# Performance work log

Measured on AMD Instinct MI355X. Metric: run time of the kernel, lower is better.

## Reference

```python
import jax, jax.numpy as jnp
import numpy as np

NUM_EMBEDDINGS = 8192
EMBEDDING_DIM = 256


def setup_inputs() -> dict:
    key = jax.random.key(0)
    kx, kw = jax.random.split(key)
    x = jax.random.normal(kx, (16384, EMBEDDING_DIM), dtype=jnp.float32)
    # nn.Embedding weight initialized uniform(-1/K, 1/K)
    bound = 1.0 / NUM_EMBEDDINGS
    weight = jax.random.uniform(kw, (NUM_EMBEDDINGS, EMBEDDING_DIM),
                                dtype=jnp.float32, minval=-bound, maxval=bound)
    return {"x": x, "weight": weight}


def reference(x, weight):
    # flatten to (N, D)
    flat_x = x.reshape(-1, EMBEDDING_DIM)
    distances = (jnp.sum(flat_x * flat_x, axis=1, keepdims=True)
                 + jnp.sum(weight * weight, axis=1)
                 - 2.0 * jnp.matmul(flat_x, weight.T))
    encoding_indices = jnp.argmin(distances, axis=1)  # (N,)
    quantized = weight[encoding_indices].reshape(x.shape)
    return quantized, encoding_indices
```

## Files before the change

### kernel.cpp

```cpp
#include <hip/hip_runtime.h>
#include <hip/hip_bf16.h>

#define NROWS 16384
#define NCODES 8192
#define DIM 256
#define BM 128
#define CPB 4096
#define CAP 24
#define MARGIN 3.0e-4f

typedef __attribute__((ext_vector_type(8))) short bf16x8;
typedef __attribute__((ext_vector_type(4))) float f32x4;

__device__ inline unsigned short f2bf(float f) {
    union { __hip_bfloat16 h; unsigned short u; } cv;
    cv.h = __float2bfloat16(f);
    return cv.u;
}
__device__ inline unsigned f2ord(float f) {
    unsigned u = __float_as_uint(f);
    return u ^ ((u >> 31) ? 0xFFFFFFFFu : 0x80000000u);
}
__device__ inline float ord2f(unsigned u) {
    unsigned v = (u & 0x80000000u) ? (u ^ 0x80000000u) : ~u;
    return __uint_as_float(v);
}

__device__ float pairwise256_sq(const float4* p) {
    float res[2];
    #pragma unroll
    for (int h = 0; h < 2; ++h) {
        float r[8];
        #pragma unroll
        for (int j = 0; j < 8; ++j) r[j] = 0.0f;
        #pragma unroll
        for (int g = 0; g < 16; ++g) {
            float4 v0 = p[h * 32 + g * 2];
            float4 v1 = p[h * 32 + g * 2 + 1];
            r[0] = __fadd_rn(r[0], __fmul_rn(v0.x, v0.x));
            r[1] = __fadd_rn(r[1], __fmul_rn(v0.y, v0.y));
            r[2] = __fadd_rn(r[2], __fmul_rn(v0.z, v0.z));
            r[3] = __fadd_rn(r[3], __fmul_rn(v0.w, v0.w));
            r[4] = __fadd_rn(r[4], __fmul_rn(v1.x, v1.x));
            r[5] = __fadd_rn(r[5], __fmul_rn(v1.y, v1.y));
            r[6] = __fadd_rn(r[6], __fmul_rn(v1.z, v1.z));
            r[7] = __fadd_rn(r[7], __fmul_rn(v1.w, v1.w));
        }
        res[h] = __fadd_rn(__fadd_rn(__fadd_rn(r[0], r[1]), __fadd_rn(r[2], r[3])),
                           __fadd_rn(__fadd_rn(r[4], r[5]), __fadd_rn(r[6], r[7])));
    }
    return __fadd_rn(res[0], res[1]);
}

__global__ __launch_bounds__(256) void sq_kernel(const float* __restrict__ x,
                                                 const float* __restrict__ w,
                                                 float* __restrict__ xsq,
                                                 float* __restrict__ wsq) {
    int gid = blockIdx.x * 256 + threadIdx.x;
    if (gid < NROWS)
        xsq[gid] = pairwise256_sq(reinterpret_cast<const float4*>(x + (size_t)gid * DIM));
    else
        wsq[gid - NROWS] =
            pairwise256_sq(reinterpret_cast<const float4*>(w + (size_t)(gid - NROWS) * DIM));
}

__global__ __launch_bounds__(256) void wfrag_kernel(const float* __restrict__ w,
                                                    unsigned short* __restrict__ whf) {
    int tid = blockIdx.x * 256 + threadIdx.x;
    int L = tid & 63;
    int rest = tid >> 6;
    int c16 = rest & 511;
    int k32 = rest >> 9;
    int code = c16 * 16 + (L & 15);
    int k = k32 * 32 + (L >> 4) * 8;
    const float4* p = reinterpret_cast<const float4*>(w + (size_t)code * DIM + k);
    float4 u0 = p[0], u1 = p[1];
    unsigned short tmp[8];
    tmp[0] = f2bf(u0.x); tmp[1] = f2bf(u0.y); tmp[2] = f2bf(u0.z); tmp[3] = f2bf(u0.w);
    tmp[4] = f2bf(u1.x); tmp[5] = f2bf(u1.y); tmp[6] = f2bf(u1.z); tmp[7] = f2bf(u1.w);
    *reinterpret_cast<uint4*>(whf + (size_t)tid * 8) = *reinterpret_cast<uint4*>(tmp);
}

__global__ __launch_bounds__(512, 2)
void vq_main(const float* __restrict__ x, const float* __restrict__ w,
             const unsigned short* __restrict__ whf,
             const float* __restrict__ wsq, const float* __restrict__ xsq,
             unsigned long long* __restrict__ best64g) {
    __shared__ unsigned short afrag[8 * 8 * 64 * 8];
    __shared__ unsigned rowmin[BM];
    __shared__ int cnt[BM];
    __shared__ int cand[BM][CAP];

    const int tid = threadIdx.x;
    const int lane = tid & 63;
    const int wv = tid >> 6;
    const int lm = lane & 15;
    const int lq = lane >> 4;

    const int blk = blockIdx.x;
    const int xcd = blk & 7;
    const int split = xcd & 1;
    const int rowGroup = (xcd >> 1) * 32 + (blk >> 3);
    const int rowBase = rowGroup * BM;
    const int codeBase = split * CPB;

    if (tid < BM) { rowmin[tid] = 0xFFFFFFFFu; cnt[tid] = 0; }

    {
        const int rg = wv;
        const float* xr = x + (size_t)(rowBase + rg * 16 + lm) * DIM + lq * 8;
        #pragma unroll
        for (int k32 = 0; k32 < 8; ++k32) {
            float4 u0 = *reinterpret_cast<const float4*>(xr + k32 * 32);
            float4 u1 = *reinterpret_cast<const float4*>(xr + k32 * 32 + 4);
            unsigned short t8[8];
            t8[0] = f2bf(u0.x); t8[1] = f2bf(u0.y); t8[2] = f2bf(u0.z); t8[3] = f2bf(u0.w);
            t8[4] = f2bf(u1.x); t8[5] = f2bf(u1.y); t8[6] = f2bf(u1.z); t8[7] = f2bf(u1.w);
            *reinterpret_cast<uint4*>(afrag + ((rg * 8 + k32) * 64 + lane) * 8) =
                *reinterpret_cast<uint4*>(t8);
        }
    }
    __syncthreads();

    const int waveCode16 = (codeBase + wv * 512) >> 4;

    for (int p = 0; p < 8; ++p) {
        const int pbase16 = waveCode16 + p * 4;
        f32x4 acc[8][4];
        #pragma unroll
        for (int rg = 0; rg < 8; ++rg)
            #pragma unroll
            for (int cf = 0; cf < 4; ++cf)
                acc[rg][cf] = (f32x4){0.f, 0.f, 0.f, 0.f};

        bf16x8 bb[2][4];
        #pragma unroll
        for (int cf = 0; cf < 4; ++cf)
            bb[0][cf] = *reinterpret_cast<const bf16x8*>(
                whf + (((size_t)(pbase16 + cf)) * 64 + lane) * 8);

        #pragma unroll
        for (int k32 = 0; k32 < 8; ++k32) {
            const int cur = k32 & 1;
            if (k32 < 7) {
                #pragma unroll
                for (int cf = 0; cf < 4; ++cf)
                    bb[cur ^ 1][cf] = *reinterpret_cast<const bf16x8*>(
                        whf + (((size_t)((k32 + 1) * 512 + pbase16 + cf)) * 64 + lane) * 8);
            }
            bf16x8 a[8];
            #pragma unroll
            for (int rg = 0; rg < 8; ++rg)
                a[rg] = *reinterpret_cast<const bf16x8*>(
                    afrag + ((rg * 8 + k32) * 64 + lane) * 8);
            #pragma unroll
            for (int cf = 0; cf < 4; ++cf)
                #pragma unroll
                for (int rg = 0; rg < 8; ++rg)
                    acc[rg][cf] = __builtin_amdgcn_mfma_f32_16x16x32_bf16(
                        a[rg], bb[cur][cf], acc[rg][cf], 0, 0, 0);
        }

        float wq[4];
        #pragma unroll
        for (int cf = 0; cf < 4; ++cf)
            wq[cf] = wsq[(pbase16 + cf) * 16 + lm];

        float mloc[32];
        #pragma unroll
        for (int rg = 0; rg < 8; ++rg) {
            #pragma unroll
            for (int r = 0; r < 4; ++r) {
                float m = __builtin_huge_valf();
                #pragma unroll
                for (int cf = 0; cf < 4; ++cf)
                    m = fminf(m, fmaf(-2.f, acc[rg][cf][r], wq[cf]));
                mloc[rg * 4 + r] = m;
                float rm = m;
                rm = fminf(rm, __shfl_xor(rm, 1, 64));
                rm = fminf(rm, __shfl_xor(rm, 2, 64));
                rm = fminf(rm, __shfl_xor(rm, 4, 64));
                rm = fminf(rm, __shfl_xor(rm, 8, 64));
                if (lm == 0)
                    atomicMin(&rowmin[rg * 16 + lq * 4 + r], f2ord(rm));
            }
        }
        #pragma unroll
        for (int rg = 0; rg < 8; ++rg) {
            #pragma unroll
            for (int r = 0; r < 4; ++r) {
                const int row = rg * 16 + lq * 4 + r;
                float limit = ord2f(rowmin[row]) + MARGIN;
                if (mloc[rg * 4 + r] <= limit) {
                    #pragma unroll
                    for (int cf = 0; cf < 4; ++cf) {
                        float s = fmaf(-2.f, acc[rg][cf][r], wq[cf]);
                        if (s <= limit) {
                            int pos = atomicAdd(&cnt[row], 1);
                            if (pos < CAP)
                                cand[row][pos] = (pbase16 + cf) * 16 + lm;
                        }
                    }
                }
            }
        }
    }
    __syncthreads();

    for (int slot = tid; slot < BM * CAP; slot += 512) {
        int row = slot / CAP, pos = slot - (slot / CAP) * CAP;
        int n = cnt[row] < CAP ? cnt[row] : CAP;
        if (pos < n) {
            int c = cand[row][pos];
            const float* xr = x + (size_t)(rowBase + row) * DIM;
            const float* wr = w + (size_t)c * DIM;
            float d = 0.f;
            for (int k = 0; k < DIM; k += 4) {
                float4 a = *reinterpret_cast<const float4*>(xr + k);
                float4 b = *reinterpret_cast<const float4*>(wr + k);
                d = fmaf(a.x, b.x, d);
                d = fmaf(a.y, b.y, d);
                d = fmaf(a.z, b.z, d);
                d = fmaf(a.w, b.w, d);
            }
            float t1 = __fadd_rn(xsq[rowBase + row], wsq[c]);
            float s = __fsub_rn(t1, __fadd_rn(d, d));
            unsigned long long key =
                ((unsigned long long)__float_as_uint(s) << 32) | (unsigned)c;
            atomicMin(best64g + rowBase + row, key);
        }
    }
}

__global__ __launch_bounds__(256)
void out_kernel(const float* __restrict__ w,
                const unsigned long long* __restrict__ best64g,
                float* __restrict__ out_q, float* __restrict__ out_idx) {
    int r = blockIdx.x * 4 + (threadIdx.x >> 6);
    int lane = threadIdx.x & 63;
    unsigned long long key = best64g[r];
    int idx = (int)(key & 0xFFFFFFFFu);
    float4 v = reinterpret_cast<const float4*>(w + (size_t)idx * DIM)[lane];
    reinterpret_cast<float4*>(out_q + (size_t)r * DIM)[lane] = v;
    if (lane == 0) out_idx[r] = (float)idx;
}

extern "C" void kernel_launch(void* const* d_in, const int* in_sizes, int n_in,
                              void* d_out, int out_size, void* d_ws, size_t ws_size,
                              hipStream_t stream) {
    const float* x = (const float*)d_in[0];
    const float* w = (const float*)d_in[1];
    float* out_q = (float*)d_out;
    float* out_idx = (float*)d_out + (size_t)NROWS * DIM;

    unsigned short* whf = (unsigned short*)d_ws;
    float* wsq = (float*)((char*)d_ws + (size_t)NCODES * DIM * 2);
    float* xsq = wsq + NCODES;
    unsigned long long* best64g = (unsigned long long*)(xsq + NROWS);

    wfrag_kernel<<<(NCODES * DIM / 8) / 256, 256, 0, stream>>>(w, whf);
    sq_kernel<<<(NROWS + NCODES) / 256, 256, 0, stream>>>(x, w, xsq, wsq);
    hipMemsetAsync(best64g, 0xFF, (size_t)NROWS * 8, stream);
    vq_main<<<256, 512, 0, stream>>>(x, w, whf, wsq, xsq, best64g);
    out_kernel<<<NROWS / 4, 256, 0, stream>>>(w, best64g, out_q, out_idx);
}
```

Before: 264.4 us.

## Fuse prep kernels and retile VQ main into smaller blocks with 4 code splits

Merges the bf16 weight fragment conversion, the squared-norm computation and the best-index initialisation into one prep kernel, replacing two launches and a memset. The squared norms now use 16 lanes per row with shuffle reduction instead of one thread per row. The main kernel drops to 64-row, 256-thread blocks and splits the codebook four ways, giving 1024 blocks instead of 256 with lower per-block LDS and register use. This raises occupancy and parallelism, but each codebook fragment is now reused across fewer rows, so B-matrix reads from global memory increase. The norm reduction order also changes, which could shift tie-breaking slightly.

```diff
diff --git a/kernel.cpp b/kernel.cpp
--- a/kernel.cpp
+++ b/kernel.cpp
@@ -4,10 +4,14 @@
 #define NROWS 16384
 #define NCODES 8192
 #define DIM 256
-#define BM 128
-#define CPB 4096
+#define BM 64
+#define SPLITS 4
+#define CPB (NCODES / SPLITS)
 #define CAP 24
 #define MARGIN 3.0e-4f
+
+#define WFRAG_BLOCKS 1024
+#define SQ_BLOCKS 1536
 
 typedef __attribute__((ext_vector_type(8))) short bf16x8;
 typedef __attribute__((ext_vector_type(4))) float f32x4;
@@ -26,67 +30,58 @@
     return __uint_as_float(v);
 }
 
-__device__ float pairwise256_sq(const float4* p) {
-    float res[2];
-    #pragma unroll
-    for (int h = 0; h < 2; ++h) {
-        float r[8];
-        #pragma unroll
-        for (int j = 0; j < 8; ++j) r[j] = 0.0f;
+__global__ __launch_bounds__(256)
+void prep_kernel(const float* __restrict__ x, const float* __restrict__ w,
+                 unsigned short* __restrict__ whf,
+                 float* __restrict__ xsq, float* __restrict__ wsq,
+                 unsigned long long* __restrict__ best64g) {
+    if (blockIdx.x < WFRAG_BLOCKS) {
+        int tid = blockIdx.x * 256 + threadIdx.x;
+        int L = tid & 63;
+        int rest = tid >> 6;
+        int c16 = rest & 511;
+        int k32 = rest >> 9;
+        int code = c16 * 16 + (L & 15);
+        int k = k32 * 32 + (L >> 4) * 8;
+        const float4* p = reinterpret_cast<const float4*>(w + (size_t)code * DIM + k);
+        float4 u0 = p[0], u1 = p[1];
+        unsigned short tmp[8];
+        tmp[0] = f2bf(u0.x); tmp[1] = f2bf(u0.y); tmp[2] = f2bf(u0.z); tmp[3] = f2bf(u0.w);
+        tmp[4] = f2bf(u1.x); tmp[5] = f2bf(u1.y); tmp[6] = f2bf(u1.z); tmp[7] = f2bf(u1.w);
+        *reinterpret_cast<uint4*>(whf + (size_t)tid * 8) = *reinterpret_cast<uint4*>(tmp);
+    } else {
+        int blk = blockIdx.x - WFRAG_BLOCKS;
+        int row = blk * 16 + (threadIdx.x >> 4);
+        int c = threadIdx.x & 15;
+        int j = c & 7, h = c >> 3;
+        const float* src = (row < NROWS) ? (x + (size_t)row * DIM)
+                                         : (w + (size_t)(row - NROWS) * DIM);
+        const float* base = src + h * 128 + j;
+        float r = 0.0f;
         #pragma unroll
         for (int g = 0; g < 16; ++g) {
-            float4 v0 = p[h * 32 + g * 2];
-            float4 v1 = p[h * 32 + g * 2 + 1];
-            r[0] = __fadd_rn(r[0], __fmul_rn(v0.x, v0.x));
-            r[1] = __fadd_rn(r[1], __fmul_rn(v0.y, v0.y));
-            r[2] = __fadd_rn(r[2], __fmul_rn(v0.z, v0.z));
-            r[3] = __fadd_rn(r[3], __fmul_rn(v0.w, v0.w));
-            r[4] = __fadd_rn(r[4], __fmul_rn(v1.x, v1.x));
-            r[5] = __fadd_rn(r[5], __fmul_rn(v1.y, v1.y));
-            r[6] = __fadd_rn(r[6], __fmul_rn(v1.z, v1.z));
-            r[7] = __fadd_rn(r[7], __fmul_rn(v1.w, v1.w));
-        }
-        res[h] = __fadd_rn(__fadd_rn(__fadd_rn(r[0], r[1]), __fadd_rn(r[2], r[3])),
-                           __fadd_rn(__fadd_rn(r[4], r[5]), __fadd_rn(r[6], r[7])));
-    }
-    return __fadd_rn(res[0], res[1]);
-}
-
-__global__ __launch_bounds__(256) void sq_kernel(const float* __restrict__ x,
-                                                 const float* __restrict__ w,
-                                                 float* __restrict__ xsq,
-                                                 float* __restrict__ wsq) {
-    int gid = blockIdx.x * 256 + threadIdx.x;
-    if (gid < NROWS)
-        xsq[gid] = pairwise256_sq(reinterpret_cast<const float4*>(x + (size_t)gid * DIM));
-    else
-        wsq[gid - NROWS] =
-            pairwise256_sq(reinterpret_cast<const float4*>(w + (size_t)(gid - NROWS) * DIM));
-}
-
-__global__ __launch_bounds__(256) void wfrag_kernel(const float* __restrict__ w,
-                                                    unsigned short* __restrict__ whf) {
-    int tid = blockIdx.x * 256 + threadIdx.x;
-    int L = tid & 63;
-    int rest = tid >> 6;
-    int c16 = rest & 511;
-    int k32 = rest >> 9;
-    int code = c16 * 16 + (L & 15);
-    int k = k32 * 32 + (L >> 4) * 8;
-    const float4* p = reinterpret_cast<const float4*>(w + (size_t)code * DIM + k);
-    float4 u0 = p[0], u1 = p[1];
-    unsigned short tmp[8];
-    tmp[0] = f2bf(u0.x); tmp[1] = f2bf(u0.y); tmp[2] = f2bf(u0.z); tmp[3] = f2bf(u0.w);
-    tmp[4] = f2bf(u1.x); tmp[5] = f2bf(u1.y); tmp[6] = f2bf(u1.z); tmp[7] = f2bf(u1.w);
-    *reinterpret_cast<uint4*>(whf + (size_t)tid * 8) = *reinterpret_cast<uint4*>(tmp);
-}
-
-__global__ __launch_bounds__(512, 2)
+            float v = base[g * 8];
+            r = __fadd_rn(r, __fmul_rn(v, v));
+        }
+        float t;
+        t = __shfl_xor(r, 1, 64); r = __fadd_rn(r, t);
+        t = __shfl_xor(r, 2, 64); r = __fadd_rn(r, t);
+        t = __shfl_xor(r, 4, 64); r = __fadd_rn(r, t);
+        t = __shfl_xor(r, 8, 64); r = __fadd_rn(r, t);
+        if (c == 0) {
+            if (row < NROWS) xsq[row] = r;
+            else wsq[row - NROWS] = r;
+        }
+        if (c == 1 && row < NROWS) best64g[row] = 0xFFFFFFFFFFFFFFFFULL;
+    }
+}
+
+__global__ __launch_bounds__(256, 3)
 void vq_main(const float* __restrict__ x, const float* __restrict__ w,
              const unsigned short* __restrict__ whf,
              const float* __restrict__ wsq, const float* __restrict__ xsq,
              unsigned long long* __restrict__ best64g) {
-    __shared__ unsigned short afrag[8 * 8 * 64 * 8];
+    __shared__ unsigned short afrag[4 * 8 * 64 * 8];
     __shared__ unsigned rowmin[BM];
     __shared__ int cnt[BM];
     __shared__ int cand[BM][CAP];
@@ -99,8 +94,8 @@
 
     const int blk = blockIdx.x;
     const int xcd = blk & 7;
-    const int split = xcd & 1;
-    const int rowGroup = (xcd >> 1) * 32 + (blk >> 3);
+    const int split = xcd & 3;
+    const int rowGroup = (xcd >> 2) * 128 + (blk >> 3);
     const int rowBase = rowGroup * BM;
     const int codeBase = split * CPB;
 
@@ -122,16 +117,21 @@
     }
     __syncthreads();
 
-    const int waveCode16 = (codeBase + wv * 512) >> 4;
+    const int waveCode16 = (codeBase >> 4) + wv * 32;
 
     for (int p = 0; p < 8; ++p) {
         const int pbase16 = waveCode16 + p * 4;
-        f32x4 acc[8][4];
-        #pragma unroll
-        for (int rg = 0; rg < 8; ++rg)
+        f32x4 acc[4][4];
+        #pragma unroll
+        for (int rg = 0; rg < 4; ++rg)
             #pragma unroll
             for (int cf = 0; cf < 4; ++cf)
                 acc[rg][cf] = (f32x4){0.f, 0.f, 0.f, 0.f};
+
+        float wq[4];
+        #pragma unroll
+        for (int cf = 0; cf < 4; ++cf)
+            wq[cf] = wsq[(pbase16 + cf) * 16 + lm];
 
         bf16x8 bb[2][4];
         #pragma unroll
@@ -148,27 +148,22 @@
                     bb[cur ^ 1][cf] = *reinterpret_cast<const bf16x8*>(
                         whf + (((size_t)((k32 + 1) * 512 + pbase16 + cf)) * 64 + lane) * 8);
             }
-            bf16x8 a[8];
-            #pragma unroll
-            for (int rg = 0; rg < 8; ++rg)
+            bf16x8 a[4];
+            #pragma unroll
+            for (int rg = 0; rg < 4; ++rg)
                 a[rg] = *reinterpret_cast<const bf16x8*>(
                     afrag + ((rg * 8 + k32) * 64 + lane) * 8);
             #pragma unroll
             for (int cf = 0; cf < 4; ++cf)
                 #pragma unroll
-                for (int rg = 0; rg < 8; ++rg)
+                for (int rg = 0; rg < 4; ++rg)
                     acc[rg][cf] = __builtin_amdgcn_mfma_f32_16x16x32_bf16(
                         a[rg], bb[cur][cf], acc[rg][cf], 0, 0, 0);
         }
 
-        float wq[4];
-        #pragma unroll
-        for (int cf = 0; cf < 4; ++cf)
-            wq[cf] = wsq[(pbase16 + cf) * 16 + lm];
-
-        float mloc[32];
-        #pragma unroll
-        for (int rg = 0; rg < 8; ++rg) {
+        float mloc[16];
+        #pragma unroll
+        for (int rg = 0; rg < 4; ++rg) {
             #pragma unroll
             for (int r = 0; r < 4; ++r) {
                 float m = __builtin_huge_valf();
@@ -186,7 +181,7 @@
             }
         }
         #pragma unroll
-        for (int rg = 0; rg < 8; ++rg) {
+        for (int rg = 0; rg < 4; ++rg) {
             #pragma unroll
             for (int r = 0; r < 4; ++r) {
                 const int row = rg * 16 + lq * 4 + r;
@@ -207,7 +202,7 @@
     }
     __syncthreads();
 
-    for (int slot = tid; slot < BM * CAP; slot += 512) {
+    for (int slot = tid; slot < BM * CAP; slot += 256) {
         int row = slot / CAP, pos = slot - (slot / CAP) * CAP;
         int n = cnt[row] < CAP ? cnt[row] : CAP;
         if (pos < n) {
@@ -258,9 +253,7 @@
     float* xsq = wsq + NCODES;
     unsigned long long* best64g = (unsigned long long*)(xsq + NROWS);
 
-    wfrag_kernel<<<(NCODES * DIM / 8) / 256, 256, 0, stream>>>(w, whf);
-    sq_kernel<<<(NROWS + NCODES) / 256, 256, 0, stream>>>(x, w, xsq, wsq);
-    hipMemsetAsync(best64g, 0xFF, (size_t)NROWS * 8, stream);
-    vq_main<<<256, 512, 0, stream>>>(x, w, whf, wsq, xsq, best64g);
+    prep_kernel<<<WFRAG_BLOCKS + SQ_BLOCKS, 256, 0, stream>>>(x, w, whf, xsq, wsq, best64g);
+    vq_main<<<(NROWS / BM) * SPLITS, 256, 0, stream>>>(x, w, whf, wsq, xsq, best64g);
     out_kernel<<<NROWS / 4, 256, 0, stream>>>(w, best64g, out_q, out_idx);
 }
```

Result: slower. 332.0 us (+25.6%).
